# Kernel tuning notes

Measured on AMD Instinct MI355X. Metric: run time of the kernel, lower is better.

Reference implementation:

```python
import jax, jax.numpy as jnp
import numpy as np


def setup_inputs() -> dict:
    key = jax.random.key(0)
    k1, k2 = jax.random.split(key)
    x = jax.random.normal(k1, (32, 64, 32, 32), dtype=jnp.float32)
    codebook = jax.random.normal(k2, (2048, 64), dtype=jnp.float32)
    return {"x": x, "codebook": codebook}


def reference(x, codebook):
    B, C, H, W = x.shape
    # (B, C, H, W) -> (B*H*W, C) channels-last flatten
    xf = jnp.transpose(x, (0, 2, 3, 1)).reshape(-1, C)
    d2 = (jnp.sum(xf * xf, axis=-1, keepdims=True)
          + jnp.sum(codebook * codebook, axis=-1)[None, :]
          - 2.0 * jnp.einsum('nc,kc->nk', xf, codebook))
    idx = jnp.argmin(d2, axis=-1)            # (B*H*W,)
    quant = codebook[idx]                    # (B*H*W, C)
    commitment_loss = jnp.mean((jax.lax.stop_gradient(quant) - xf) ** 2)
    codebook_loss = jnp.mean((quant - jax.lax.stop_gradient(xf)) ** 2)
    # Straight-through estimator
    quant_ste = xf + jax.lax.stop_gradient(quant - xf)
    quant_out = jnp.transpose(quant_ste.reshape(B, H, W, C), (0, 3, 1, 2))
    min_encoding_indices = idx.reshape(B, H, W)
    return quant_out, codebook_loss, commitment_loss, min_encoding_indices
```

## Files before the change

kernel.cpp:

```cpp
#include <hip/hip_runtime.h>

#define NROWS    32768
#define KENT     2048
#define OUT_Q_SZ 2097152
#define N_ELEMS  2097152.0f
#define THRG     1e-4f
#define KLO      0.0009765625f

typedef _Float16 f16x8  __attribute__((ext_vector_type(8)));
typedef float    f32x16 __attribute__((ext_vector_type(16)));

#define WS_EN    1024
#define WS_ENH   9216
#define WS_LIST  20480
#define WS_CBH   262144
#define WS_CBL   524288

__global__ __launch_bounds__(256) void vq_prep_kernel(
    const float* __restrict__ cb, float* __restrict__ ws)
{
    const int unit = blockIdx.x * 256 + threadIdx.x;
    if (unit == 0) { ws[0] = 0.0f; ((unsigned*)ws)[1] = 0u; }

    const int gm = unit >> 8, ks = (unit >> 6) & 3, l = unit & 63;
    const int e  = gm * 32 + (l & 31);
    const int ch = ks * 16 + ((l >> 5) << 3);
    float4 v0 = *(const float4*)(cb + e * 64 + ch);
    float4 v1 = *(const float4*)(cb + e * 64 + ch + 4);
    float vv[8] = {v0.x,v0.y,v0.z,v0.w, v1.x,v1.y,v1.z,v1.w};
    f16x8 h, lo;
#pragma unroll
    for (int j = 0; j < 8; ++j) {
        _Float16 hi = (_Float16)vv[j];
        float r = (vv[j] - (float)hi) * 1024.0f;
        h[j] = hi; lo[j] = (_Float16)r;
    }
    *(f16x8*)((_Float16*)((char*)ws + WS_CBH) + (size_t)unit * 8) = h;
    *(f16x8*)((_Float16*)((char*)ws + WS_CBL) + (size_t)unit * 8) = lo;

    if (unit < KENT) {
        const float4* row = (const float4*)(cb + unit * 64);
        float s = 0.0f;
#pragma unroll
        for (int i = 0; i < 16; ++i) {
            float4 v = row[i];
            s += v.x * v.x + v.y * v.y + v.z * v.z + v.w * v.w;
        }
        *((float*)((char*)ws + WS_EN) + unit) = s;
        int ein = unit & 31;
        int half = (ein >> 2) & 1;
        int r = (ein & 3) + ((ein >> 3) << 2);
        *((float*)((char*)ws + WS_ENH) + (unit & ~31) + half * 16 + r) = -0.5f * s;
    }
}

__global__ __launch_bounds__(512, 2) void vq_main_kernel(
    const float* __restrict__ x, const float* __restrict__ cb,
    float* __restrict__ ws, float* __restrict__ out_q,
    float* __restrict__ out_idx)
{
    __shared__ float lds_x[64 * 132];
    __shared__ float mb1[128 * 4], mb2[128 * 4];
    __shared__ int   mbi[128 * 4];
    __shared__ int   idx_s[128], flag_s[128];
    __shared__ float wp[8];

    const float*    enhp = (const float*)((char*)ws + WS_ENH);
    const _Float16* cbh  = (const _Float16*)((char*)ws + WS_CBH);
    const _Float16* cbl  = (const _Float16*)((char*)ws + WS_CBL);
    unsigned* cnt  = (unsigned*)ws + 1;
    unsigned* list = (unsigned*)((char*)ws + WS_LIST);

    const int tid = threadIdx.x, bid = blockIdx.x;
    const int n0  = bid * 128;
    const int b   = n0 >> 10;
    const int hw0 = n0 & 1023;
    const float* xg = x + b * 65536 + hw0;

#pragma unroll
    for (int it = 0; it < 4; ++it) {
        int f = it * 512 + tid;
        int c = f >> 5, seg = f & 31;
        float4 v = *(const float4*)(xg + c * 1024 + seg * 4);
        *(float4*)(&lds_x[c * 132 + seg * 4]) = v;
    }
    __syncthreads();

    const int l   = tid & 63;
    const int wv  = tid >> 6;
    const int rgp = wv >> 2;
    const int eq  = wv & 3;
    const int r0  = rgp * 64;

    f16x8 bh[2][4], bl[2][4];
#pragma unroll
    for (int s = 0; s < 2; ++s)
#pragma unroll
        for (int ks = 0; ks < 4; ++ks) {
            f16x8 h, lo;
#pragma unroll
            for (int j = 0; j < 8; ++j) {
                int ch = ks * 16 + ((l >> 5) << 3) + j;
                float f = lds_x[ch * 132 + r0 + s * 32 + (l & 31)];
                _Float16 hi = (_Float16)f;
                float r = (f - (float)hi) * 1024.0f;
                h[j] = hi; lo[j] = (_Float16)r;
            }
            bh[s][ks] = h; bl[s][ks] = lo;
        }

    float m1[2][4], m2[2][4]; int bx[2][4];
#pragma unroll
    for (int s = 0; s < 2; ++s)
#pragma unroll
        for (int t = 0; t < 4; ++t) { m1[s][t] = -3.4e38f; m2[s][t] = -3.4e38f; bx[s][t] = 0; }

#pragma unroll 2
    for (int m = 0; m < 16; ++m) {
        const _Float16* ap = cbh + ((size_t)((eq * 16 + m) * 4) * 64 + l) * 8;
        const _Float16* lp = cbl + ((size_t)((eq * 16 + m) * 4) * 64 + l) * 8;
        f16x8 ah0 = *(const f16x8*)(ap);
        f16x8 ah1 = *(const f16x8*)(ap + 512);
        f16x8 ah2 = *(const f16x8*)(ap + 1024);
        f16x8 ah3 = *(const f16x8*)(ap + 1536);
        f16x8 al0 = *(const f16x8*)(lp);
        f16x8 al1 = *(const f16x8*)(lp + 512);
        f16x8 al2 = *(const f16x8*)(lp + 1024);
        f16x8 al3 = *(const f16x8*)(lp + 1536);

        f32x16 aA;
        {
            const float4* ep4 = (const float4*)(enhp + eq * 512 + m * 32 + ((l >> 5) << 4));
            float4 q0 = ep4[0], q1 = ep4[1], q2 = ep4[2], q3 = ep4[3];
            aA[0]=q0.x; aA[1]=q0.y; aA[2]=q0.z; aA[3]=q0.w;
            aA[4]=q1.x; aA[5]=q1.y; aA[6]=q1.z; aA[7]=q1.w;
            aA[8]=q2.x; aA[9]=q2.y; aA[10]=q2.z; aA[11]=q2.w;
            aA[12]=q3.x; aA[13]=q3.y; aA[14]=q3.z; aA[15]=q3.w;
        }
        f32x16 aB = aA;
        f32x16 cA = {0.f,0.f,0.f,0.f,0.f,0.f,0.f,0.f,0.f,0.f,0.f,0.f,0.f,0.f,0.f,0.f};
        f32x16 cB = cA;

        aA = __builtin_amdgcn_mfma_f32_32x32x16_f16(ah0, bh[0][0], aA, 0, 0, 0);
        aB = __builtin_amdgcn_mfma_f32_32x32x16_f16(ah0, bh[1][0], aB, 0, 0, 0);
        cA = __builtin_amdgcn_mfma_f32_32x32x16_f16(ah0, bl[0][0], cA, 0, 0, 0);
        cB = __builtin_amdgcn_mfma_f32_32x32x16_f16(ah0, bl[1][0], cB, 0, 0, 0);
        aA = __builtin_amdgcn_mfma_f32_32x32x16_f16(ah1, bh[0][1], aA, 0, 0, 0);
        aB = __builtin_amdgcn_mfma_f32_32x32x16_f16(ah1, bh[1][1], aB, 0, 0, 0);
        cA = __builtin_amdgcn_mfma_f32_32x32x16_f16(ah1, bl[0][1], cA, 0, 0, 0);
        cB = __builtin_amdgcn_mfma_f32_32x32x16_f16(ah1, bl[1][1], cB, 0, 0, 0);
        aA = __builtin_amdgcn_mfma_f32_32x32x16_f16(ah2, bh[0][2], aA, 0, 0, 0);
        aB = __builtin_amdgcn_mfma_f32_32x32x16_f16(ah2, bh[1][2], aB, 0, 0, 0);
        cA = __builtin_amdgcn_mfma_f32_32x32x16_f16(ah2, bl[0][2], cA, 0, 0, 0);
        cB = __builtin_amdgcn_mfma_f32_32x32x16_f16(ah2, bl[1][2], cB, 0, 0, 0);
        aA = __builtin_amdgcn_mfma_f32_32x32x16_f16(ah3, bh[0][3], aA, 0, 0, 0);
        aB = __builtin_amdgcn_mfma_f32_32x32x16_f16(ah3, bh[1][3], aB, 0, 0, 0);
        cA = __builtin_amdgcn_mfma_f32_32x32x16_f16(ah3, bl[0][3], cA, 0, 0, 0);
        cB = __builtin_amdgcn_mfma_f32_32x32x16_f16(ah3, bl[1][3], cB, 0, 0, 0);
        cA = __builtin_amdgcn_mfma_f32_32x32x16_f16(al0, bh[0][0], cA, 0, 0, 0);
        cB = __builtin_amdgcn_mfma_f32_32x32x16_f16(al0, bh[1][0], cB, 0, 0, 0);
        cA = __builtin_amdgcn_mfma_f32_32x32x16_f16(al1, bh[0][1], cA, 0, 0, 0);
        cB = __builtin_amdgcn_mfma_f32_32x32x16_f16(al1, bh[1][1], cB, 0, 0, 0);
        cA = __builtin_amdgcn_mfma_f32_32x32x16_f16(al2, bh[0][2], cA, 0, 0, 0);
        cB = __builtin_amdgcn_mfma_f32_32x32x16_f16(al2, bh[1][2], cB, 0, 0, 0);
        cA = __builtin_amdgcn_mfma_f32_32x32x16_f16(al3, bh[0][3], cA, 0, 0, 0);
        cB = __builtin_amdgcn_mfma_f32_32x32x16_f16(al3, bh[1][3], cB, 0, 0, 0);

        const int ebl = eq * 512 + m * 32 + ((l >> 5) << 2);
#pragma unroll
        for (int r = 0; r < 16; ++r) {
            int t = r >> 2;
            int ent = ebl + ((r >> 2) << 3) + (r & 3);
            float gA = fmaf(cA[r], KLO, aA[r]);
            bool  tA = gA > m1[0][t];
            m2[0][t] = __builtin_amdgcn_fmed3f(gA, m1[0][t], m2[0][t]);
            m1[0][t] = fmaxf(gA, m1[0][t]);
            bx[0][t] = tA ? ent : bx[0][t];
            float gB = fmaf(cB[r], KLO, aB[r]);
            bool  tB = gB > m1[1][t];
            m2[1][t] = __builtin_amdgcn_fmed3f(gB, m1[1][t], m2[1][t]);
            m1[1][t] = fmaxf(gB, m1[1][t]);
            bx[1][t] = tB ? ent : bx[1][t];
        }
    }

#pragma unroll
    for (int s = 0; s < 2; ++s) {
        float v1 = m1[s][0], v2 = m2[s][0]; int ix = bx[s][0];
#pragma unroll
        for (int t = 1; t < 4; ++t) {
            bool gt = (m1[s][t] > v1) || (m1[s][t] == v1 && bx[s][t] < ix);
            float loser = gt ? v1 : m1[s][t];
            v1 = gt ? m1[s][t] : v1;
            ix = gt ? bx[s][t] : ix;
            v2 = fmaxf(loser, fmaxf(v2, m2[s][t]));
        }
        float o1 = __shfl_xor(v1, 32, 64);
        float o2 = __shfl_xor(v2, 32, 64);
        int   oi = __shfl_xor(ix, 32, 64);
        bool gt = (o1 > v1) || (o1 == v1 && oi < ix);
        float loser = gt ? v1 : o1;
        v1 = gt ? o1 : v1; ix = gt ? oi : ix;
        v2 = fmaxf(loser, fmaxf(v2, o2));
        if (l < 32) {
            int row = r0 + s * 32 + l;
            mb1[row * 4 + eq] = v1;
            mb2[row * 4 + eq] = v2;
            mbi[row * 4 + eq] = ix;
        }
    }
    __syncthreads();

    if (tid < 128) {
        float v1 = -3.4e38f, v2 = -3.4e38f; int ix = 0;
#pragma unroll
        for (int q = 0; q < 4; ++q) {
            float o1 = mb1[tid * 4 + q];
            float o2 = mb2[tid * 4 + q];
            int   oi = mbi[tid * 4 + q];
            bool gt = (o1 > v1) || (o1 == v1 && oi < ix);
            float loser = gt ? v1 : o1;
            v1 = gt ? o1 : v1; ix = gt ? oi : ix;
            v2 = fmaxf(loser, fmaxf(v2, o2));
        }
        out_idx[n0 + tid] = (float)ix;
        int fl = (v1 - v2) <= THRG;
        idx_s[tid] = ix; flag_s[tid] = fl;
        if (fl) { unsigned p = atomicAdd(cnt, 1u); list[p] = n0 + tid; }
    }
    __syncthreads();

    float lsum = 0.0f;
#pragma unroll
    for (int it = 0; it < 16; ++it) {
        int e = it * 512 + tid;
        int c = e >> 7, r = e & 127;
        float q  = cb[idx_s[r] * 64 + c];
        float xv = lds_x[c * 132 + r];
        out_q[(b << 16) + (c << 10) + hw0 + r] = xv + (q - xv);
        float df = q - xv;
        lsum += flag_s[r] ? 0.0f : df * df;
    }
#pragma unroll
    for (int mm = 1; mm < 64; mm <<= 1) lsum += __shfl_xor(lsum, mm, 64);
    if (l == 0) wp[wv] = lsum;
    __syncthreads();
    if (tid == 0) {
        float s = 0.0f;
#pragma unroll
        for (int w = 0; w < 8; ++w) s += wp[w];
        atomicAdd(ws, s);
    }
}

__global__ __launch_bounds__(256) void vq_fallback_kernel(
    const float* __restrict__ x, const float* __restrict__ cb,
    float* __restrict__ ws, float* __restrict__ out_q, float* __restrict__ out_idx)
{
    __shared__ float x_s[64];
    __shared__ float rd[256];
    __shared__ int   ri[256];

    const float* en = (const float*)((char*)ws + WS_EN);
    const unsigned F = *(const unsigned*)((char*)ws + 4);
    const unsigned* list = (const unsigned*)((char*)ws + WS_LIST);
    const int t = threadIdx.x;

    for (unsigned li = blockIdx.x; li < F; li += gridDim.x) {
        int row = list[li];
        int b = row >> 10, hw = row & 1023;
        if (t < 64) x_s[t] = x[(b << 16) + (t << 10) + hw];
        __syncthreads();

        float best = 3.4e38f; int bi = 0;
#pragma unroll 1
        for (int i = 0; i < 8; ++i) {
            int e = i * 256 + t;
            float dot = 0.0f;
#pragma unroll
            for (int c4 = 0; c4 < 16; ++c4) {
                float4 cv = *(const float4*)(cb + e * 64 + c4 * 4);
                float4 xv = *(const float4*)&x_s[c4 * 4];
                dot += cv.x * xv.x + cv.y * xv.y + cv.z * xv.z + cv.w * xv.w;
            }
            float d = en[e] - 2.0f * dot;
            if (d < best) { best = d; bi = e; }
        }
        rd[t] = best; ri[t] = bi;
        __syncthreads();
        for (int s = 128; s > 0; s >>= 1) {
            if (t < s) {
                bool lt = (rd[t + s] < rd[t]) ||
                          (rd[t + s] == rd[t] && ri[t + s] < ri[t]);
                if (lt) { rd[t] = rd[t + s]; ri[t] = ri[t + s]; }
            }
            __syncthreads();
        }
        int ix = ri[0];
        if (t == 0) out_idx[row] = (float)ix;
        if (t < 64) {
            float q = cb[ix * 64 + t];
            float xv = x_s[t];
            out_q[(b << 16) + (t << 10) + hw] = xv + (q - xv);
            float df = q - xv;
            float ls = df * df;
#pragma unroll
            for (int mm = 1; mm < 64; mm <<= 1) ls += __shfl_xor(ls, mm, 64);
            if (t == 0) atomicAdd(ws, ls);
        }
        __syncthreads();
    }
}

__global__ void vq_finalize_kernel(const float* __restrict__ ws, float* __restrict__ out) {
    float m = ws[0] * (1.0f / N_ELEMS);
    out[OUT_Q_SZ]     = m;
    out[OUT_Q_SZ + 1] = m;
}

extern "C" void kernel_launch(void* const* d_in, const int* in_sizes, int n_in,
                              void* d_out, int out_size, void* d_ws, size_t ws_size,
                              hipStream_t stream) {
    const float* x  = (const float*)d_in[0];
    const float* cb = (const float*)d_in[1];
    float* out  = (float*)d_out;
    float* ws   = (float*)d_ws;
    float* oidx = out + OUT_Q_SZ + 2;

    vq_prep_kernel<<<64, 256, 0, stream>>>(cb, ws);
    vq_main_kernel<<<256, 512, 0, stream>>>(x, cb, ws, out, oidx);
    vq_fallback_kernel<<<64, 256, 0, stream>>>(x, cb, ws, out, oidx);
    vq_finalize_kernel<<<1, 1, 0, stream>>>(ws, out);
}
```

Baseline: 68.10 us.

## Software-pipeline codebook fragment loads, stage norms in LDS, fuse finalize into fallback

The main loop now prefetches the next codebook tile's fp16 hi/lo fragments into a second register set while computing the current tile, hiding global load latency behind MFMA work. The per-entry -0.5*||e||^2 table is copied into shared memory once per block instead of being read from global memory on every iteration. The separate finalize kernel launch is removed: the last fallback block to finish, found through an atomic counter, writes the loss means. The double-buffered fragments raise register pressure under the 2-blocks-per-CU launch bound, and the last-block pattern depends on fences and a counter that is reset in the prep kernel.

```diff
diff --git a/kernel.cpp b/kernel.cpp
--- a/kernel.cpp
+++ b/kernel.cpp
@@ -20,7 +20,7 @@
     const float* __restrict__ cb, float* __restrict__ ws)
 {
     const int unit = blockIdx.x * 256 + threadIdx.x;
-    if (unit == 0) { ws[0] = 0.0f; ((unsigned*)ws)[1] = 0u; }
+    if (unit == 0) { ws[0] = 0.0f; ((unsigned*)ws)[1] = 0u; ((unsigned*)ws)[2] = 0u; }
 
     const int gm = unit >> 8, ks = (unit >> 6) & 3, l = unit & 63;
     const int e  = gm * 32 + (l & 31);
@@ -54,20 +54,89 @@
     }
 }
 
+#define LOAD_FRAGS(A0,A1,A2,A3,L0,L1,L2,L3, GM) do {                    \
+    const _Float16* ap_ = cbh + ((size_t)((GM) * 4) * 64 + l) * 8;      \
+    const _Float16* lp_ = cbl + ((size_t)((GM) * 4) * 64 + l) * 8;      \
+    A0 = *(const f16x8*)(ap_);                                          \
+    A1 = *(const f16x8*)(ap_ + 512);                                    \
+    A2 = *(const f16x8*)(ap_ + 1024);                                   \
+    A3 = *(const f16x8*)(ap_ + 1536);                                   \
+    L0 = *(const f16x8*)(lp_);                                          \
+    L1 = *(const f16x8*)(lp_ + 512);                                    \
+    L2 = *(const f16x8*)(lp_ + 1024);                                   \
+    L3 = *(const f16x8*)(lp_ + 1536);                                   \
+} while (0)
+
+#define COMPUTE_TILE(H0,H1,H2,H3,Q0,Q1,Q2,Q3, M) do {                          \
+    f32x16 aA;                                                                 \
+    {                                                                          \
+        const float4* ep4_ = (const float4*)(&enh_s[eq * 512 + (M) * 32 + ((l >> 5) << 4)]); \
+        float4 q0=ep4_[0], q1=ep4_[1], q2=ep4_[2], q3=ep4_[3];                 \
+        aA[0]=q0.x; aA[1]=q0.y; aA[2]=q0.z; aA[3]=q0.w;                        \
+        aA[4]=q1.x; aA[5]=q1.y; aA[6]=q1.z; aA[7]=q1.w;                        \
+        aA[8]=q2.x; aA[9]=q2.y; aA[10]=q2.z; aA[11]=q2.w;                      \
+        aA[12]=q3.x; aA[13]=q3.y; aA[14]=q3.z; aA[15]=q3.w;                    \
+    }                                                                          \
+    f32x16 aB = aA;                                                            \
+    f32x16 cA = {0.f,0.f,0.f,0.f,0.f,0.f,0.f,0.f,0.f,0.f,0.f,0.f,0.f,0.f,0.f,0.f}; \
+    f32x16 cB = cA;                                                            \
+    aA = __builtin_amdgcn_mfma_f32_32x32x16_f16(H0, bh[0][0], aA, 0, 0, 0);    \
+    aB = __builtin_amdgcn_mfma_f32_32x32x16_f16(H0, bh[1][0], aB, 0, 0, 0);    \
+    cA = __builtin_amdgcn_mfma_f32_32x32x16_f16(H0, bl[0][0], cA, 0, 0, 0);    \
+    cB = __builtin_amdgcn_mfma_f32_32x32x16_f16(H0, bl[1][0], cB, 0, 0, 0);    \
+    aA = __builtin_amdgcn_mfma_f32_32x32x16_f16(H1, bh[0][1], aA, 0, 0, 0);    \
+    aB = __builtin_amdgcn_mfma_f32_32x32x16_f16(H1, bh[1][1], aB, 0, 0, 0);    \
+    cA = __builtin_amdgcn_mfma_f32_32x32x16_f16(H1, bl[0][1], cA, 0, 0, 0);    \
+    cB = __builtin_amdgcn_mfma_f32_32x32x16_f16(H1, bl[1][1], cB, 0, 0, 0);    \
+    aA = __builtin_amdgcn_mfma_f32_32x32x16_f16(H2, bh[0][2], aA, 0, 0, 0);    \
+    aB = __builtin_amdgcn_mfma_f32_32x32x16_f16(H2, bh[1][2], aB, 0, 0, 0);    \
+    cA = __builtin_amdgcn_mfma_f32_32x32x16_f16(H2, bl[0][2], cA, 0, 0, 0);    \
+    cB = __builtin_amdgcn_mfma_f32_32x32x16_f16(H2, bl[1][2], cB, 0, 0, 0);    \
+    aA = __builtin_amdgcn_mfma_f32_32x32x16_f16(H3, bh[0][3], aA, 0, 0, 0);    \
+    aB = __builtin_amdgcn_mfma_f32_32x32x16_f16(H3, bh[1][3], aB, 0, 0, 0);    \
+    cA = __builtin_amdgcn_mfma_f32_32x32x16_f16(H3, bl[0][3], cA, 0, 0, 0);    \
+    cB = __builtin_amdgcn_mfma_f32_32x32x16_f16(H3, bl[1][3], cB, 0, 0, 0);    \
+    cA = __builtin_amdgcn_mfma_f32_32x32x16_f16(Q0, bh[0][0], cA, 0, 0, 0);    \
+    cB = __builtin_amdgcn_mfma_f32_32x32x16_f16(Q0, bh[1][0], cB, 0, 0, 0);    \
+    cA = __builtin_amdgcn_mfma_f32_32x32x16_f16(Q1, bh[0][1], cA, 0, 0, 0);    \
+    cB = __builtin_amdgcn_mfma_f32_32x32x16_f16(Q1, bh[1][1], cB, 0, 0, 0);    \
+    cA = __builtin_amdgcn_mfma_f32_32x32x16_f16(Q2, bh[0][2], cA, 0, 0, 0);    \
+    cB = __builtin_amdgcn_mfma_f32_32x32x16_f16(Q2, bh[1][2], cB, 0, 0, 0);    \
+    cA = __builtin_amdgcn_mfma_f32_32x32x16_f16(Q3, bh[0][3], cA, 0, 0, 0);    \
+    cB = __builtin_amdgcn_mfma_f32_32x32x16_f16(Q3, bh[1][3], cB, 0, 0, 0);    \
+    const int ebl_ = eq * 512 + (M) * 32 + ((l >> 5) << 2);                    \
+    _Pragma("unroll")                                                          \
+    for (int r = 0; r < 16; ++r) {                                             \
+        int t = r >> 2;                                                        \
+        int ent = ebl_ + ((r >> 2) << 3) + (r & 3);                            \
+        float gA = fmaf(cA[r], KLO, aA[r]);                                    \
+        bool  tA = gA > m1[0][t];                                              \
+        m2[0][t] = __builtin_amdgcn_fmed3f(gA, m1[0][t], m2[0][t]);            \
+        m1[0][t] = fmaxf(gA, m1[0][t]);                                        \
+        bx[0][t] = tA ? ent : bx[0][t];                                        \
+        float gB = fmaf(cB[r], KLO, aB[r]);                                    \
+        bool  tB = gB > m1[1][t];                                              \
+        m2[1][t] = __builtin_amdgcn_fmed3f(gB, m1[1][t], m2[1][t]);            \
+        m1[1][t] = fmaxf(gB, m1[1][t]);                                        \
+        bx[1][t] = tB ? ent : bx[1][t];                                        \
+    }                                                                          \
+} while (0)
+
 __global__ __launch_bounds__(512, 2) void vq_main_kernel(
     const float* __restrict__ x, const float* __restrict__ cb,
     float* __restrict__ ws, float* __restrict__ out_q,
     float* __restrict__ out_idx)
 {
     __shared__ float lds_x[64 * 132];
+    __shared__ float enh_s[2048];
     __shared__ float mb1[128 * 4], mb2[128 * 4];
     __shared__ int   mbi[128 * 4];
     __shared__ int   idx_s[128], flag_s[128];
     __shared__ float wp[8];
 
-    const float*    enhp = (const float*)((char*)ws + WS_ENH);
     const _Float16* cbh  = (const _Float16*)((char*)ws + WS_CBH);
     const _Float16* cbl  = (const _Float16*)((char*)ws + WS_CBL);
+    const float*    enhp = (const float*)((char*)ws + WS_ENH);
     unsigned* cnt  = (unsigned*)ws + 1;
     unsigned* list = (unsigned*)((char*)ws + WS_LIST);
 
@@ -84,6 +153,8 @@
         float4 v = *(const float4*)(xg + c * 1024 + seg * 4);
         *(float4*)(&lds_x[c * 132 + seg * 4]) = v;
     }
+#pragma unroll
+    for (int i = tid; i < 2048; i += 512) enh_s[i] = enhp[i];
     __syncthreads();
 
     const int l   = tid & 63;
@@ -115,73 +186,18 @@
 #pragma unroll
         for (int t = 0; t < 4; ++t) { m1[s][t] = -3.4e38f; m2[s][t] = -3.4e38f; bx[s][t] = 0; }
 
-#pragma unroll 2
-    for (int m = 0; m < 16; ++m) {
-        const _Float16* ap = cbh + ((size_t)((eq * 16 + m) * 4) * 64 + l) * 8;
-        const _Float16* lp = cbl + ((size_t)((eq * 16 + m) * 4) * 64 + l) * 8;
-        f16x8 ah0 = *(const f16x8*)(ap);
-        f16x8 ah1 = *(const f16x8*)(ap + 512);
-        f16x8 ah2 = *(const f16x8*)(ap + 1024);
-        f16x8 ah3 = *(const f16x8*)(ap + 1536);
-        f16x8 al0 = *(const f16x8*)(lp);
-        f16x8 al1 = *(const f16x8*)(lp + 512);
-        f16x8 al2 = *(const f16x8*)(lp + 1024);
-        f16x8 al3 = *(const f16x8*)(lp + 1536);
-
-        f32x16 aA;
-        {
-            const float4* ep4 = (const float4*)(enhp + eq * 512 + m * 32 + ((l >> 5) << 4));
-            float4 q0 = ep4[0], q1 = ep4[1], q2 = ep4[2], q3 = ep4[3];
-            aA[0]=q0.x; aA[1]=q0.y; aA[2]=q0.z; aA[3]=q0.w;
-            aA[4]=q1.x; aA[5]=q1.y; aA[6]=q1.z; aA[7]=q1.w;
-            aA[8]=q2.x; aA[9]=q2.y; aA[10]=q2.z; aA[11]=q2.w;
-            aA[12]=q3.x; aA[13]=q3.y; aA[14]=q3.z; aA[15]=q3.w;
-        }
-        f32x16 aB = aA;
-        f32x16 cA = {0.f,0.f,0.f,0.f,0.f,0.f,0.f,0.f,0.f,0.f,0.f,0.f,0.f,0.f,0.f,0.f};
-        f32x16 cB = cA;
-
-        aA = __builtin_amdgcn_mfma_f32_32x32x16_f16(ah0, bh[0][0], aA, 0, 0, 0);
-        aB = __builtin_amdgcn_mfma_f32_32x32x16_f16(ah0, bh[1][0], aB, 0, 0, 0);
-        cA = __builtin_amdgcn_mfma_f32_32x32x16_f16(ah0, bl[0][0], cA, 0, 0, 0);
-        cB = __builtin_amdgcn_mfma_f32_32x32x16_f16(ah0, bl[1][0], cB, 0, 0, 0);
-        aA = __builtin_amdgcn_mfma_f32_32x32x16_f16(ah1, bh[0][1], aA, 0, 0, 0);
-        aB = __builtin_amdgcn_mfma_f32_32x32x16_f16(ah1, bh[1][1], aB, 0, 0, 0);
-        cA = __builtin_amdgcn_mfma_f32_32x32x16_f16(ah1, bl[0][1], cA, 0, 0, 0);
-        cB = __builtin_amdgcn_mfma_f32_32x32x16_f16(ah1, bl[1][1], cB, 0, 0, 0);
-        aA = __builtin_amdgcn_mfma_f32_32x32x16_f16(ah2, bh[0][2], aA, 0, 0, 0);
-        aB = __builtin_amdgcn_mfma_f32_32x32x16_f16(ah2, bh[1][2], aB, 0, 0, 0);
-        cA = __builtin_amdgcn_mfma_f32_32x32x16_f16(ah2, bl[0][2], cA, 0, 0, 0);
-        cB = __builtin_amdgcn_mfma_f32_32x32x16_f16(ah2, bl[1][2], cB, 0, 0, 0);
-        aA = __builtin_amdgcn_mfma_f32_32x32x16_f16(ah3, bh[0][3], aA, 0, 0, 0);
-        aB = __builtin_amdgcn_mfma_f32_32x32x16_f16(ah3, bh[1][3], aB, 0, 0, 0);
-        cA = __builtin_amdgcn_mfma_f32_32x32x16_f16(ah3, bl[0][3], cA, 0, 0, 0);
-        cB = __builtin_amdgcn_mfma_f32_32x32x16_f16(ah3, bl[1][3], cB, 0, 0, 0);
-        cA = __builtin_amdgcn_mfma_f32_32x32x16_f16(al0, bh[0][0], cA, 0, 0, 0);
-        cB = __builtin_amdgcn_mfma_f32_32x32x16_f16(al0, bh[1][0], cB, 0, 0, 0);
-        cA = __builtin_amdgcn_mfma_f32_32x32x16_f16(al1, bh[0][1], cA, 0, 0, 0);
-        cB = __builtin_amdgcn_mfma_f32_32x32x16_f16(al1, bh[1][1], cB, 0, 0, 0);
-        cA = __builtin_amdgcn_mfma_f32_32x32x16_f16(al2, bh[0][2], cA, 0, 0, 0);
-        cB = __builtin_amdgcn_mfma_f32_32x32x16_f16(al2, bh[1][2], cB, 0, 0, 0);
-        cA = __builtin_amdgcn_mfma_f32_32x32x16_f16(al3, bh[0][3], cA, 0, 0, 0);
-        cB = __builtin_amdgcn_mfma_f32_32x32x16_f16(al3, bh[1][3], cB, 0, 0, 0);
-
-        const int ebl = eq * 512 + m * 32 + ((l >> 5) << 2);
-#pragma unroll
-        for (int r = 0; r < 16; ++r) {
-            int t = r >> 2;
-            int ent = ebl + ((r >> 2) << 3) + (r & 3);
-            float gA = fmaf(cA[r], KLO, aA[r]);
-            bool  tA = gA > m1[0][t];
-            m2[0][t] = __builtin_amdgcn_fmed3f(gA, m1[0][t], m2[0][t]);
-            m1[0][t] = fmaxf(gA, m1[0][t]);
-            bx[0][t] = tA ? ent : bx[0][t];
-            float gB = fmaf(cB[r], KLO, aB[r]);
-            bool  tB = gB > m1[1][t];
-            m2[1][t] = __builtin_amdgcn_fmed3f(gB, m1[1][t], m2[1][t]);
-            m1[1][t] = fmaxf(gB, m1[1][t]);
-            bx[1][t] = tB ? ent : bx[1][t];
-        }
+    f16x8 pa0, pa1, pa2, pa3, pl0, pl1, pl2, pl3;
+    f16x8 qa0, qa1, qa2, qa3, ql0, ql1, ql2, ql3;
+    LOAD_FRAGS(pa0,pa1,pa2,pa3,pl0,pl1,pl2,pl3, eq * 16);
+
+#pragma unroll 1
+    for (int m = 0; m < 16; m += 2) {
+        int g1 = eq * 16 + ((m + 1) & 15);
+        LOAD_FRAGS(qa0,qa1,qa2,qa3,ql0,ql1,ql2,ql3, g1);
+        COMPUTE_TILE(pa0,pa1,pa2,pa3,pl0,pl1,pl2,pl3, m);
+        int g2 = eq * 16 + ((m + 2) & 15);
+        LOAD_FRAGS(pa0,pa1,pa2,pa3,pl0,pl1,pl2,pl3, g2);
+        COMPUTE_TILE(qa0,qa1,qa2,qa3,ql0,ql1,ql2,ql3, m + 1);
     }
 
 #pragma unroll
@@ -260,10 +276,12 @@
     __shared__ float x_s[64];
     __shared__ float rd[256];
     __shared__ int   ri[256];
+    __shared__ unsigned lastflag;
 
     const float* en = (const float*)((char*)ws + WS_EN);
     const unsigned F = *(const unsigned*)((char*)ws + 4);
     const unsigned* list = (const unsigned*)((char*)ws + WS_LIST);
+    unsigned* done = (unsigned*)ws + 2;
     const int t = threadIdx.x;
 
     for (unsigned li = blockIdx.x; li < F; li += gridDim.x) {
@@ -310,12 +328,15 @@
         }
         __syncthreads();
     }
-}
-
-__global__ void vq_finalize_kernel(const float* __restrict__ ws, float* __restrict__ out) {
-    float m = ws[0] * (1.0f / N_ELEMS);
-    out[OUT_Q_SZ]     = m;
-    out[OUT_Q_SZ + 1] = m;
+
+    __threadfence();
+    if (t == 0) lastflag = atomicAdd(done, 1u);
+    __syncthreads();
+    if (lastflag == gridDim.x - 1 && t == 0) {
+        float m = (*(volatile float*)ws) * (1.0f / N_ELEMS);
+        out_q[OUT_Q_SZ]     = m;
+        out_q[OUT_Q_SZ + 1] = m;
+    }
 }
 
 extern "C" void kernel_launch(void* const* d_in, const int* in_sizes, int n_in,
@@ -330,5 +351,4 @@
     vq_prep_kernel<<<64, 256, 0, stream>>>(cb, ws);
     vq_main_kernel<<<256, 512, 0, stream>>>(x, cb, ws, out, oidx);
     vq_fallback_kernel<<<64, 256, 0, stream>>>(x, cb, ws, out, oidx);
-    vq_finalize_kernel<<<1, 1, 0, stream>>>(ws, out);
 }
```

Result: slower. 72.49 us (+6.5%).

## Halve rows per block, stage norms in LDS, fold finalize into fallback

Applied to the files above, without the earlier changes.

The main kernel now handles 64 rows per block instead of 128, launching 512 blocks with a higher launch-bounds occupancy target. The per-wave register tile and MFMA count are halved, and the codebook norm bias is staged in shared memory instead of read from global memory. The finalize kernel is removed: the last fallback block, detected with an atomic counter, writes the loss means, saving one launch. The tradeoff is that each block now re-streams the full fp16 codebook for half as many rows, doubling codebook traffic.

```diff
diff --git a/kernel.cpp b/kernel.cpp
--- a/kernel.cpp
+++ b/kernel.cpp
@@ -20,7 +20,7 @@
     const float* __restrict__ cb, float* __restrict__ ws)
 {
     const int unit = blockIdx.x * 256 + threadIdx.x;
-    if (unit == 0) { ws[0] = 0.0f; ((unsigned*)ws)[1] = 0u; }
+    if (unit == 0) { ws[0] = 0.0f; ((unsigned*)ws)[1] = 0u; ((unsigned*)ws)[2] = 0u; }
 
     const int gm = unit >> 8, ks = (unit >> 6) & 3, l = unit & 63;
     const int e  = gm * 32 + (l & 31);
@@ -54,71 +54,71 @@
     }
 }
 
-__global__ __launch_bounds__(512, 2) void vq_main_kernel(
+__global__ __launch_bounds__(512, 4) void vq_main_kernel(
     const float* __restrict__ x, const float* __restrict__ cb,
     float* __restrict__ ws, float* __restrict__ out_q,
     float* __restrict__ out_idx)
 {
-    __shared__ float lds_x[64 * 132];
-    __shared__ float mb1[128 * 4], mb2[128 * 4];
-    __shared__ int   mbi[128 * 4];
-    __shared__ int   idx_s[128], flag_s[128];
+    __shared__ float lds_x[64 * 68];
+    __shared__ float enh_s[2048];
+    __shared__ float mb1[64 * 4], mb2[64 * 4];
+    __shared__ int   mbi[64 * 4];
+    __shared__ int   idx_s[64], flag_s[64];
     __shared__ float wp[8];
 
-    const float*    enhp = (const float*)((char*)ws + WS_ENH);
     const _Float16* cbh  = (const _Float16*)((char*)ws + WS_CBH);
     const _Float16* cbl  = (const _Float16*)((char*)ws + WS_CBL);
+    const float*    enhp = (const float*)((char*)ws + WS_ENH);
     unsigned* cnt  = (unsigned*)ws + 1;
     unsigned* list = (unsigned*)((char*)ws + WS_LIST);
 
     const int tid = threadIdx.x, bid = blockIdx.x;
-    const int n0  = bid * 128;
+    const int n0  = bid * 64;
     const int b   = n0 >> 10;
     const int hw0 = n0 & 1023;
     const float* xg = x + b * 65536 + hw0;
 
-#pragma unroll
-    for (int it = 0; it < 4; ++it) {
-        int f = it * 512 + tid;
-        int c = f >> 5, seg = f & 31;
-        float4 v = *(const float4*)(xg + c * 1024 + seg * 4);
-        *(float4*)(&lds_x[c * 132 + seg * 4]) = v;
-    }
+    {
+        int c = tid >> 3, seg = tid & 7;
+        float4 a0 = *(const float4*)(xg + c * 1024 + seg * 8);
+        float4 a1 = *(const float4*)(xg + c * 1024 + seg * 8 + 4);
+        *(float4*)(&lds_x[c * 68 + seg * 8])     = a0;
+        *(float4*)(&lds_x[c * 68 + seg * 8 + 4]) = a1;
+    }
+#pragma unroll
+    for (int i = tid; i < 2048; i += 512) enh_s[i] = enhp[i];
     __syncthreads();
 
     const int l   = tid & 63;
     const int wv  = tid >> 6;
     const int rgp = wv >> 2;
     const int eq  = wv & 3;
-    const int r0  = rgp * 64;
-
-    f16x8 bh[2][4], bl[2][4];
-#pragma unroll
-    for (int s = 0; s < 2; ++s)
-#pragma unroll
-        for (int ks = 0; ks < 4; ++ks) {
-            f16x8 h, lo;
-#pragma unroll
-            for (int j = 0; j < 8; ++j) {
-                int ch = ks * 16 + ((l >> 5) << 3) + j;
-                float f = lds_x[ch * 132 + r0 + s * 32 + (l & 31)];
-                _Float16 hi = (_Float16)f;
-                float r = (f - (float)hi) * 1024.0f;
-                h[j] = hi; lo[j] = (_Float16)r;
-            }
-            bh[s][ks] = h; bl[s][ks] = lo;
-        }
-
-    float m1[2][4], m2[2][4]; int bx[2][4];
-#pragma unroll
-    for (int s = 0; s < 2; ++s)
-#pragma unroll
-        for (int t = 0; t < 4; ++t) { m1[s][t] = -3.4e38f; m2[s][t] = -3.4e38f; bx[s][t] = 0; }
+    const int r0  = rgp * 32;
+
+    f16x8 bh[4], bl[4];
+#pragma unroll
+    for (int ks = 0; ks < 4; ++ks) {
+        f16x8 h, lo;
+#pragma unroll
+        for (int j = 0; j < 8; ++j) {
+            int ch = ks * 16 + ((l >> 5) << 3) + j;
+            float f = lds_x[ch * 68 + r0 + (l & 31)];
+            _Float16 hi = (_Float16)f;
+            float r = (f - (float)hi) * 1024.0f;
+            h[j] = hi; lo[j] = (_Float16)r;
+        }
+        bh[ks] = h; bl[ks] = lo;
+    }
+
+    float m1[4], m2[4]; int bx[4];
+#pragma unroll
+    for (int t = 0; t < 4; ++t) { m1[t] = -3.4e38f; m2[t] = -3.4e38f; bx[t] = 0; }
 
 #pragma unroll 2
     for (int m = 0; m < 16; ++m) {
-        const _Float16* ap = cbh + ((size_t)((eq * 16 + m) * 4) * 64 + l) * 8;
-        const _Float16* lp = cbl + ((size_t)((eq * 16 + m) * 4) * 64 + l) * 8;
+        const int gm = eq * 16 + m;
+        const _Float16* ap = cbh + ((size_t)(gm * 4) * 64 + l) * 8;
+        const _Float16* lp = cbl + ((size_t)(gm * 4) * 64 + l) * 8;
         f16x8 ah0 = *(const f16x8*)(ap);
         f16x8 ah1 = *(const f16x8*)(ap + 512);
         f16x8 ah2 = *(const f16x8*)(ap + 1024);
@@ -130,41 +130,27 @@
 
         f32x16 aA;
         {
-            const float4* ep4 = (const float4*)(enhp + eq * 512 + m * 32 + ((l >> 5) << 4));
+            const float4* ep4 = (const float4*)(&enh_s[eq * 512 + m * 32 + ((l >> 5) << 4)]);
             float4 q0 = ep4[0], q1 = ep4[1], q2 = ep4[2], q3 = ep4[3];
             aA[0]=q0.x; aA[1]=q0.y; aA[2]=q0.z; aA[3]=q0.w;
             aA[4]=q1.x; aA[5]=q1.y; aA[6]=q1.z; aA[7]=q1.w;
             aA[8]=q2.x; aA[9]=q2.y; aA[10]=q2.z; aA[11]=q2.w;
             aA[12]=q3.x; aA[13]=q3.y; aA[14]=q3.z; aA[15]=q3.w;
         }
-        f32x16 aB = aA;
         f32x16 cA = {0.f,0.f,0.f,0.f,0.f,0.f,0.f,0.f,0.f,0.f,0.f,0.f,0.f,0.f,0.f,0.f};
-        f32x16 cB = cA;
-
-        aA = __builtin_amdgcn_mfma_f32_32x32x16_f16(ah0, bh[0][0], aA, 0, 0, 0);
-        aB = __builtin_amdgcn_mfma_f32_32x32x16_f16(ah0, bh[1][0], aB, 0, 0, 0);
-        cA = __builtin_amdgcn_mfma_f32_32x32x16_f16(ah0, bl[0][0], cA, 0, 0, 0);
-        cB = __builtin_amdgcn_mfma_f32_32x32x16_f16(ah0, bl[1][0], cB, 0, 0, 0);
-        aA = __builtin_amdgcn_mfma_f32_32x32x16_f16(ah1, bh[0][1], aA, 0, 0, 0);
-        aB = __builtin_amdgcn_mfma_f32_32x32x16_f16(ah1, bh[1][1], aB, 0, 0, 0);
-        cA = __builtin_amdgcn_mfma_f32_32x32x16_f16(ah1, bl[0][1], cA, 0, 0, 0);
-        cB = __builtin_amdgcn_mfma_f32_32x32x16_f16(ah1, bl[1][1], cB, 0, 0, 0);
-        aA = __builtin_amdgcn_mfma_f32_32x32x16_f16(ah2, bh[0][2], aA, 0, 0, 0);
-        aB = __builtin_amdgcn_mfma_f32_32x32x16_f16(ah2, bh[1][2], aB, 0, 0, 0);
-        cA = __builtin_amdgcn_mfma_f32_32x32x16_f16(ah2, bl[0][2], cA, 0, 0, 0);
-        cB = __builtin_amdgcn_mfma_f32_32x32x16_f16(ah2, bl[1][2], cB, 0, 0, 0);
-        aA = __builtin_amdgcn_mfma_f32_32x32x16_f16(ah3, bh[0][3], aA, 0, 0, 0);
-        aB = __builtin_amdgcn_mfma_f32_32x32x16_f16(ah3, bh[1][3], aB, 0, 0, 0);
-        cA = __builtin_amdgcn_mfma_f32_32x32x16_f16(ah3, bl[0][3], cA, 0, 0, 0);
-        cB = __builtin_amdgcn_mfma_f32_32x32x16_f16(ah3, bl[1][3], cB, 0, 0, 0);
-        cA = __builtin_amdgcn_mfma_f32_32x32x16_f16(al0, bh[0][0], cA, 0, 0, 0);
-        cB = __builtin_amdgcn_mfma_f32_32x32x16_f16(al0, bh[1][0], cB, 0, 0, 0);
-        cA = __builtin_amdgcn_mfma_f32_32x32x16_f16(al1, bh[0][1], cA, 0, 0, 0);
-        cB = __builtin_amdgcn_mfma_f32_32x32x16_f16(al1, bh[1][1], cB, 0, 0, 0);
-        cA = __builtin_amdgcn_mfma_f32_32x32x16_f16(al2, bh[0][2], cA, 0, 0, 0);
-        cB = __builtin_amdgcn_mfma_f32_32x32x16_f16(al2, bh[1][2], cB, 0, 0, 0);
-        cA = __builtin_amdgcn_mfma_f32_32x32x16_f16(al3, bh[0][3], cA, 0, 0, 0);
-        cB = __builtin_amdgcn_mfma_f32_32x32x16_f16(al3, bh[1][3], cB, 0, 0, 0);
+
+        aA = __builtin_amdgcn_mfma_f32_32x32x16_f16(ah0, bh[0], aA, 0, 0, 0);
+        cA = __builtin_amdgcn_mfma_f32_32x32x16_f16(ah0, bl[0], cA, 0, 0, 0);
+        aA = __builtin_amdgcn_mfma_f32_32x32x16_f16(ah1, bh[1], aA, 0, 0, 0);
+        cA = __builtin_amdgcn_mfma_f32_32x32x16_f16(ah1, bl[1], cA, 0, 0, 0);
+        aA = __builtin_amdgcn_mfma_f32_32x32x16_f16(ah2, bh[2], aA, 0, 0, 0);
+        cA = __builtin_amdgcn_mfma_f32_32x32x16_f16(ah2, bl[2], cA, 0, 0, 0);
+        aA = __builtin_amdgcn_mfma_f32_32x32x16_f16(ah3, bh[3], aA, 0, 0, 0);
+        cA = __builtin_amdgcn_mfma_f32_32x32x16_f16(ah3, bl[3], cA, 0, 0, 0);
+        cA = __builtin_amdgcn_mfma_f32_32x32x16_f16(al0, bh[0], cA, 0, 0, 0);
+        cA = __builtin_amdgcn_mfma_f32_32x32x16_f16(al1, bh[1], cA, 0, 0, 0);
+        cA = __builtin_amdgcn_mfma_f32_32x32x16_f16(al2, bh[2], cA, 0, 0, 0);
+        cA = __builtin_amdgcn_mfma_f32_32x32x16_f16(al3, bh[3], cA, 0, 0, 0);
 
         const int ebl = eq * 512 + m * 32 + ((l >> 5) << 2);
 #pragma unroll
@@ -172,28 +158,22 @@
             int t = r >> 2;
             int ent = ebl + ((r >> 2) << 3) + (r & 3);
             float gA = fmaf(cA[r], KLO, aA[r]);
-            bool  tA = gA > m1[0][t];
-            m2[0][t] = __builtin_amdgcn_fmed3f(gA, m1[0][t], m2[0][t]);
-            m1[0][t] = fmaxf(gA, m1[0][t]);
-            bx[0][t] = tA ? ent : bx[0][t];
-            float gB = fmaf(cB[r], KLO, aB[r]);
-            bool  tB = gB > m1[1][t];
-            m2[1][t] = __builtin_amdgcn_fmed3f(gB, m1[1][t], m2[1][t]);
-            m1[1][t] = fmaxf(gB, m1[1][t]);
-            bx[1][t] = tB ? ent : bx[1][t];
-        }
-    }
-
-#pragma unroll
-    for (int s = 0; s < 2; ++s) {
-        float v1 = m1[s][0], v2 = m2[s][0]; int ix = bx[s][0];
+            bool  tA = gA > m1[t];
+            m2[t] = __builtin_amdgcn_fmed3f(gA, m1[t], m2[t]);
+            m1[t] = fmaxf(gA, m1[t]);
+            bx[t] = tA ? ent : bx[t];
+        }
+    }
+
+    {
+        float v1 = m1[0], v2 = m2[0]; int ix = bx[0];
 #pragma unroll
         for (int t = 1; t < 4; ++t) {
-            bool gt = (m1[s][t] > v1) || (m1[s][t] == v1 && bx[s][t] < ix);
-            float loser = gt ? v1 : m1[s][t];
-            v1 = gt ? m1[s][t] : v1;
-            ix = gt ? bx[s][t] : ix;
-            v2 = fmaxf(loser, fmaxf(v2, m2[s][t]));
+            bool gt = (m1[t] > v1) || (m1[t] == v1 && bx[t] < ix);
+            float loser = gt ? v1 : m1[t];
+            v1 = gt ? m1[t] : v1;
+            ix = gt ? bx[t] : ix;
+            v2 = fmaxf(loser, fmaxf(v2, m2[t]));
         }
         float o1 = __shfl_xor(v1, 32, 64);
         float o2 = __shfl_xor(v2, 32, 64);
@@ -203,7 +183,7 @@
         v1 = gt ? o1 : v1; ix = gt ? oi : ix;
         v2 = fmaxf(loser, fmaxf(v2, o2));
         if (l < 32) {
-            int row = r0 + s * 32 + l;
+            int row = r0 + l;
             mb1[row * 4 + eq] = v1;
             mb2[row * 4 + eq] = v2;
             mbi[row * 4 + eq] = ix;
@@ -211,7 +191,7 @@
     }
     __syncthreads();
 
-    if (tid < 128) {
+    if (tid < 64) {
         float v1 = -3.4e38f, v2 = -3.4e38f; int ix = 0;
 #pragma unroll
         for (int q = 0; q < 4; ++q) {
@@ -232,11 +212,11 @@
 
     float lsum = 0.0f;
 #pragma unroll
-    for (int it = 0; it < 16; ++it) {
+    for (int it = 0; it < 8; ++it) {
         int e = it * 512 + tid;
-        int c = e >> 7, r = e & 127;
+        int c = e >> 6, r = e & 63;
         float q  = cb[idx_s[r] * 64 + c];
-        float xv = lds_x[c * 132 + r];
+        float xv = lds_x[c * 68 + r];
         out_q[(b << 16) + (c << 10) + hw0 + r] = xv + (q - xv);
         float df = q - xv;
         lsum += flag_s[r] ? 0.0f : df * df;
@@ -260,10 +240,12 @@
     __shared__ float x_s[64];
     __shared__ float rd[256];
     __shared__ int   ri[256];
+    __shared__ unsigned lastflag;
 
     const float* en = (const float*)((char*)ws + WS_EN);
     const unsigned F = *(const unsigned*)((char*)ws + 4);
     const unsigned* list = (const unsigned*)((char*)ws + WS_LIST);
+    unsigned* done = (unsigned*)ws + 2;
     const int t = threadIdx.x;
 
     for (unsigned li = blockIdx.x; li < F; li += gridDim.x) {
@@ -310,12 +292,15 @@
         }
         __syncthreads();
     }
-}
-
-__global__ void vq_finalize_kernel(const float* __restrict__ ws, float* __restrict__ out) {
-    float m = ws[0] * (1.0f / N_ELEMS);
-    out[OUT_Q_SZ]     = m;
-    out[OUT_Q_SZ + 1] = m;
+
+    __threadfence();
+    if (t == 0) lastflag = atomicAdd(done, 1u);
+    __syncthreads();
+    if (lastflag == gridDim.x - 1 && t == 0) {
+        float m = (*(volatile float*)ws) * (1.0f / N_ELEMS);
+        out_q[OUT_Q_SZ]     = m;
+        out_q[OUT_Q_SZ + 1] = m;
+    }
 }
 
 extern "C" void kernel_launch(void* const* d_in, const int* in_sizes, int n_in,
@@ -328,7 +313,6 @@
     float* oidx = out + OUT_Q_SZ + 2;
 
     vq_prep_kernel<<<64, 256, 0, stream>>>(cb, ws);
-    vq_main_kernel<<<256, 512, 0, stream>>>(x, cb, ws, out, oidx);
+    vq_main_kernel<<<512, 512, 0, stream>>>(x, cb, ws, out, oidx);
     vq_fallback_kernel<<<64, 256, 0, stream>>>(x, cb, ws, out, oidx);
-    vq_finalize_kernel<<<1, 1, 0, stream>>>(ws, out);
 }
```

New measurement: 80.60 us. 18.4% more time.
